# Optimization experiments

Measured on AMD Instinct MI355X. Metric: run time of the kernel, lower is better.

Reference implementation:

```python
import jax, jax.numpy as jnp
import numpy as np

N = 16384   # total gate nodes (64 graphs x 256 gates)
B = 64      # graphs in batch
E = 49152   # directed edges (avg in-degree 3)
Q = 32      # qubit_num
F = 256     # feat_dim
D = 2 * F   # node feature dim = 512
H = 2       # heads
A = 128     # action_num


def _gatv2(x, wl, wr, att, b, src, dst, n):
    # PyG GATv2Conv (concat=True, share_weights=False, negative_slope=0.2)
    h, c = att.shape
    xl = (x @ wl).reshape(n, h, c)   # source-side projection [N,H,C]
    xr = (x @ wr).reshape(n, h, c)   # target-side projection [N,H,C]
    e = jax.nn.leaky_relu(xl[src] + xr[dst], 0.2)       # [E,H,C]
    logit = jnp.einsum('ehc,hc->eh', e, att)             # [E,H]
    m = jax.ops.segment_max(logit, dst, num_segments=n)  # softmax over in-edges per target
    p = jnp.exp(logit - m[dst])
    den = jax.ops.segment_sum(p, dst, num_segments=n)
    alpha = p / den[dst]                                 # [E,H]
    out = jax.ops.segment_sum(alpha[:, :, None] * xl[src], dst, num_segments=n)
    return out.reshape(n, h * c) + b


def _forward(x, xt_w1, xt_b1, xt_w2, xt_b2,
             g0_wl, g0_wr, g0_att, g0_b,
             g1_wl, g1_wr, g1_att, g1_b,
             g2_wl, g2_wr, g2_att, g2_b,
             g3_wl, g3_wr, g3_att, g3_b,
             g4_wl, g4_wr, g4_att, g4_b,
             ln_w, ln_b, aggr_t,
             m_w1, m_b1, m_w2, m_b2, m_w3, m_b3,
             edge_index, batch):
    lr = lambda v: jax.nn.leaky_relu(v, 0.01)
    # x_trans: Linear -> LeakyReLU -> Linear, then fold qubit-pairs into one node
    h0 = lr(x @ xt_w1 + xt_b1) @ xt_w2 + xt_b2           # [2N, F]
    cx = h0.reshape(-1, D)                               # [N, 2F]
    n = cx.shape[0]
    # GATv2Conv default add_self_loops=True (inputs contain no self loops)
    sl = jnp.arange(n, dtype=edge_index.dtype)
    src = jnp.concatenate([edge_index[0], sl])
    dst = jnp.concatenate([edge_index[1], sl])
    res = cx
    h = lr(_gatv2(cx, g0_wl, g0_wr, g0_att, g0_b, src, dst, n))
    for wl_, wr_, att_, b_ in ((g1_wl, g1_wr, g1_att, g1_b),
                               (g2_wl, g2_wr, g2_att, g2_b),
                               (g3_wl, g3_wr, g3_att, g3_b)):
        h = lr(_gatv2(h, wl_, wr_, att_, b_, src, dst, n))
    h = lr(_gatv2(h, g4_wl, g4_wr, g4_att, g4_b, src, dst, n))
    h = h + res                                           # residual [N, 2F]
    # PyG LayerNorm(mode='graph'): normalize over nodes AND channels per graph
    cnt = jax.ops.segment_sum(jnp.ones((n,), h.dtype), batch, num_segments=B)
    norm = cnt * h.shape[1]
    mean = jax.ops.segment_sum(h.sum(-1), batch, num_segments=B) / norm
    hc = h - mean[batch][:, None]
    var = jax.ops.segment_sum((hc * hc).sum(-1), batch, num_segments=B) / norm
    h = hc / jnp.sqrt(var + 1e-5)[batch][:, None] * ln_w + ln_b
    # SoftmaxAggregation(learn=True): channel-wise softmax over nodes per graph
    logit = h * aggr_t
    mg = jax.ops.segment_max(logit, batch, num_segments=B)
    p = jnp.exp(logit - mg[batch])
    den = jax.ops.segment_sum(p, batch, num_segments=B)
    g = jax.ops.segment_sum((p / den[batch]) * h, batch, num_segments=B)  # [B, 2F]
    # head MLP 512->384->256->128
    o = lr(g @ m_w1 + m_b1)
    o = lr(o @ m_w2 + m_b2)
    return o @ m_w3 + m_b3


def setup_inputs() -> dict:
    key = jax.random.key(0)
    ks = iter(jax.random.split(key, 64))
    def rn(shp, s=0.05):
        return jax.random.normal(next(ks), shp, jnp.float32) * s
    d = {}
    d['x'] = jax.random.normal(next(ks), (2 * N, Q), jnp.float32)
    src = jax.random.randint(next(ks), (E,), 0, N, jnp.int32)
    off = jax.random.randint(next(ks), (E,), 1, N, jnp.int32)
    d['edge_index'] = jnp.stack([src, (src + off) % N])  # no self loops
    d['batch'] = jnp.arange(N, dtype=jnp.int32) // (N // B)
    d['xt_w1'] = rn((Q, F)); d['xt_b1'] = rn((F,))
    d['xt_w2'] = rn((F, F)); d['xt_b2'] = rn((F,))
    d['g0_wl'] = rn((D, H * D)); d['g0_wr'] = rn((D, H * D))
    d['g0_att'] = rn((H, D));    d['g0_b'] = rn((H * D,))
    for i in (1, 2, 3):
        d[f'g{i}_wl'] = rn((H * D, H * D)); d[f'g{i}_wr'] = rn((H * D, H * D))
        d[f'g{i}_att'] = rn((H, D));        d[f'g{i}_b'] = rn((H * D,))
    d['g4_wl'] = rn((H * D, D)); d['g4_wr'] = rn((H * D, D))
    d['g4_att'] = rn((1, D));    d['g4_b'] = rn((D,))
    d['ln_w'] = jnp.ones((D,), jnp.float32); d['ln_b'] = jnp.zeros((D,), jnp.float32)
    d['aggr_t'] = jnp.array(1.0, jnp.float32)
    d['m_w1'] = rn((D, 384)); d['m_b1'] = rn((384,))
    d['m_w2'] = rn((384, 256)); d['m_b2'] = rn((256,))
    d['m_w3'] = rn((256, A)); d['m_b3'] = rn((A,))
    return d


def reference(x, edge_index, batch, xt_w1, xt_b1, xt_w2, xt_b2,
              g0_wl, g0_wr, g0_att, g0_b,
              g1_wl, g1_wr, g1_att, g1_b,
              g2_wl, g2_wr, g2_att, g2_b,
              g3_wl, g3_wr, g3_att, g3_b,
              g4_wl, g4_wr, g4_att, g4_b,
              ln_w, ln_b, aggr_t,
              m_w1, m_b1, m_w2, m_b2, m_w3, m_b3):
    return _forward(x, xt_w1, xt_b1, xt_w2, xt_b2,
                    g0_wl, g0_wr, g0_att, g0_b,
                    g1_wl, g1_wr, g1_att, g1_b,
                    g2_wl, g2_wr, g2_att, g2_b,
                    g3_wl, g3_wr, g3_att, g3_b,
                    g4_wl, g4_wr, g4_att, g4_b,
                    ln_w, ln_b, aggr_t,
                    m_w1, m_b1, m_w2, m_b2, m_w3, m_b3,
                    edge_index, batch)
```

## Files before the change

kernel.cpp:

```cpp
#include <hip/hip_runtime.h>
#include <hip/hip_bf16.h>

typedef __hip_bfloat16 bf16;

#define NN 16384
#define BBG 64
#define EE 49152
#define ET (EE + NN)
#define DD 512
#define NG (NN / BBG)

__device__ __forceinline__ float b2f(bf16 v) { return __bfloat162float(v); }
__device__ __forceinline__ bf16 f2b(float v) { return __float2bfloat16(v); }
__device__ __forceinline__ float sb2f(short s) {
    unsigned u = ((unsigned)(unsigned short)s) << 16;
    return __builtin_bit_cast(float, u);
}
__device__ __forceinline__ short f2bs(float v) {
    bf16 b = f2b(v);
    return __builtin_bit_cast(short, b);
}
__device__ __forceinline__ int clampi(int v, int lo, int hi)
{
    return v < lo ? lo : (v > hi ? hi : v);
}

__device__ __forceinline__ unsigned char enc_e4m3(float y)
{
    unsigned b = __builtin_bit_cast(unsigned, y);
    unsigned s = (b >> 31) << 7;
    float a = fabsf(y);
    unsigned ab = b & 0x7fffffffu;
    unsigned rb = ab + (1u << 19);
    int e = (int)(rb >> 23) - 120;
    unsigned m = (rb >> 20) & 7u;
    unsigned qn = (unsigned)(e << 3) | m;
    if (qn > 126u) qn = 126u;
    unsigned qd = (unsigned)__float2int_rn(a * 512.f);
    unsigned q = (a < 0.015625f) ? qd : qn;
    return (unsigned char)(q | s);
}
__device__ __forceinline__ float dec_e4m3(unsigned q)
{
    unsigned e = (q >> 3) & 15u, m = q & 7u;
    float nrm = __builtin_bit_cast(float, ((e + 120u) << 23) | (m << 20));
    float dnm = (float)m * 0.001953125f;
    float v = e ? nrm : dnm;
    return (q & 128u) ? -v : v;
}

typedef __attribute__((ext_vector_type(8))) short bf16x8;
typedef __attribute__((ext_vector_type(4))) float f32x4;

#define AS1 __attribute__((address_space(1)))
#define AS3 __attribute__((address_space(3)))

__global__ __launch_bounds__(256) void gemm_mfma_bt(
    const bf16* __restrict__ A, const bf16* __restrict__ Bt,
    const float* __restrict__ bias, bf16* __restrict__ Cb,
    int M, int N, int K, float slope, int has_act)
{
    __shared__ bf16 As[128 * 32];
    __shared__ bf16 Bs[128 * 32];
    const int tid = threadIdx.x;
    const int w = tid >> 6;
    const int l = tid & 63;
    const int bm = blockIdx.y * 128;
    const int bn = blockIdx.x * 128;
    const int wrow = (w >> 1) * 64;
    const int wcol = (w & 1) * 64;
    const int quad = l >> 4;
    const int c16 = l & 15;

    const int lrow = l >> 2;
    const int lchunk = l & 3;
    const bf16* Ag = A + (size_t)(bm + w * 16 + lrow) * K + lchunk * 8;
    const bf16* Bg = Bt + (size_t)(bn + w * 16 + lrow) * K + lchunk * 8;
    char* AsB = (char*)As;
    char* BsB = (char*)Bs;

    f32x4 acc[4][4] = {};

    for (int k0 = 0; k0 < K; k0 += 32) {
        __builtin_amdgcn_global_load_lds((const AS1 void*)(Ag + k0),
            (AS3 void*)(AsB + w * 1024), 16, 0, 0);
        __builtin_amdgcn_global_load_lds((const AS1 void*)(Ag + (size_t)64 * K + k0),
            (AS3 void*)(AsB + 4096 + w * 1024), 16, 0, 0);
        __builtin_amdgcn_global_load_lds((const AS1 void*)(Bg + k0),
            (AS3 void*)(BsB + w * 1024), 16, 0, 0);
        __builtin_amdgcn_global_load_lds((const AS1 void*)(Bg + (size_t)64 * K + k0),
            (AS3 void*)(BsB + 4096 + w * 1024), 16, 0, 0);
        __syncthreads();

        bf16x8 a[4], b[4];
#pragma unroll
        for (int i = 0; i < 4; i++) {
            int ra = wrow + i * 16 + c16;
            a[i] = *(const bf16x8*)(AsB + ra * 64 + quad * 16);
            int rb = wcol + i * 16 + c16;
            b[i] = *(const bf16x8*)(BsB + rb * 64 + quad * 16);
        }
#pragma unroll
        for (int i = 0; i < 4; i++)
#pragma unroll
            for (int j = 0; j < 4; j++)
                acc[i][j] = __builtin_amdgcn_mfma_f32_16x16x32_bf16(
                    a[i], b[j], acc[i][j], 0, 0, 0);
        __syncthreads();
    }

#pragma unroll
    for (int i = 0; i < 4; i++) {
#pragma unroll
        for (int j = 0; j < 4; j++) {
            int col = bn + wcol + j * 16 + c16;
            float bv = bias ? bias[col] : 0.f;
#pragma unroll
            for (int r = 0; r < 4; r++) {
                int row = bm + wrow + i * 16 + quad * 4 + r;
                float v = acc[i][j][r] + bv;
                if (has_act) v = (v >= 0.f) ? v : v * slope;
                Cb[(size_t)row * N + col] = f2b(v);
            }
        }
    }
}

__global__ __launch_bounds__(256) void gemm_mfma_dual(
    const bf16* __restrict__ A, const bf16* __restrict__ Bt,
    bf16* __restrict__ X0, bf16* __restrict__ X1,
    int M, int K, int HC)
{
    __shared__ bf16 As[128 * 32];
    __shared__ bf16 Bs[128 * 32];
    const int tid = threadIdx.x;
    const int w = tid >> 6;
    const int l = tid & 63;
    const int bm = blockIdx.y * 128;
    const int bn = blockIdx.x * 128;
    const int wrow = (w >> 1) * 64;
    const int wcol = (w & 1) * 64;
    const int quad = l >> 4;
    const int c16 = l & 15;

    const int lrow = l >> 2;
    const int lchunk = l & 3;
    const bf16* Ag = A + (size_t)(bm + w * 16 + lrow) * K + lchunk * 8;
    const bf16* Bg = Bt + (size_t)(bn + w * 16 + lrow) * K + lchunk * 8;
    char* AsB = (char*)As;
    char* BsB = (char*)Bs;

    f32x4 acc[4][4] = {};

    for (int k0 = 0; k0 < K; k0 += 32) {
        __builtin_amdgcn_global_load_lds((const AS1 void*)(Ag + k0),
            (AS3 void*)(AsB + w * 1024), 16, 0, 0);
        __builtin_amdgcn_global_load_lds((const AS1 void*)(Ag + (size_t)64 * K + k0),
            (AS3 void*)(AsB + 4096 + w * 1024), 16, 0, 0);
        __builtin_amdgcn_global_load_lds((const AS1 void*)(Bg + k0),
            (AS3 void*)(BsB + w * 1024), 16, 0, 0);
        __builtin_amdgcn_global_load_lds((const AS1 void*)(Bg + (size_t)64 * K + k0),
            (AS3 void*)(BsB + 4096 + w * 1024), 16, 0, 0);
        __syncthreads();

        bf16x8 a[4], b[4];
#pragma unroll
        for (int i = 0; i < 4; i++) {
            int ra = wrow + i * 16 + c16;
            a[i] = *(const bf16x8*)(AsB + ra * 64 + quad * 16);
            int rb = wcol + i * 16 + c16;
            b[i] = *(const bf16x8*)(BsB + rb * 64 + quad * 16);
        }
#pragma unroll
        for (int i = 0; i < 4; i++)
#pragma unroll
            for (int j = 0; j < 4; j++)
                acc[i][j] = __builtin_amdgcn_mfma_f32_16x16x32_bf16(
                    a[i], b[j], acc[i][j], 0, 0, 0);
        __syncthreads();
    }

#pragma unroll
    for (int i = 0; i < 4; i++) {
#pragma unroll
        for (int j = 0; j < 4; j++) {
            int col = bn + wcol + j * 16 + c16;
            bf16* dst = (col < HC) ? (X0 + col) : (X1 + col - HC);
#pragma unroll
            for (int r = 0; r < 4; r++) {
                int row = bm + wrow + i * 16 + quad * 4 + r;
                dst[(size_t)row * HC] = f2b(acc[i][j][r]);
            }
        }
    }
}

__global__ __launch_bounds__(256, 4) void quant_rows(
    const bf16* __restrict__ xl, unsigned char* __restrict__ xq,
    bf16* __restrict__ xs)
{
    const int n = blockIdx.x * 4 + (threadIdx.x >> 6);
    const int lane = threadIdx.x & 63;
    const bf16* rp = xl + (size_t)n * 1024 + lane * 16;
    bf16x8 v0 = *(const bf16x8*)(rp);
    bf16x8 v1 = *(const bf16x8*)(rp + 8);
    float x[16];
#pragma unroll
    for (int k = 0; k < 8; k++) { x[k] = sb2f(v0[k]); x[8 + k] = sb2f(v1[k]); }
    float mx = 0.f;
#pragma unroll
    for (int k = 0; k < 16; k++) mx = fmaxf(mx, fabsf(x[k]));
    float sc = b2f(f2b(fmaxf(mx, 1e-20f) * (1.f / 448.f)));
    float isc = 1.f / sc;
    uint4 q;
    unsigned* qw = (unsigned*)&q;
#pragma unroll
    for (int w = 0; w < 4; w++) {
        unsigned pk = 0;
#pragma unroll
        for (int b = 0; b < 4; b++)
            pk |= ((unsigned)enc_e4m3(x[w * 4 + b] * isc)) << (b * 8);
        qw[w] = pk;
    }
    *(uint4*)(xq + (size_t)n * 1024 + lane * 16) = q;
    xs[(size_t)n * 64 + lane] = f2b(sc);
}

__global__ __launch_bounds__(256) void gemm_f32(
    const float* __restrict__ A, const float* __restrict__ W,
    const float* __restrict__ bias, float* __restrict__ C,
    int M, int N, int K, float slope, int has_act)
{
    const int BK = 16;
    __shared__ float Asm[BK][64 + 1];
    __shared__ float Wsm[BK][64 + 1];
    int tid = threadIdx.x;
    int bm = blockIdx.y * 64;
    int bn = blockIdx.x * 64;
    int tr = tid >> 4;
    int tc = tid & 15;
    float acc[4][4] = {};

    for (int k0 = 0; k0 < K; k0 += BK) {
        {
            int col = tid & 15;
            int row = tid >> 4;
#pragma unroll
            for (int p = 0; p < 4; p++) {
                int r = row + p * 16;
                Asm[col][r] = A[(size_t)(bm + r) * K + k0 + col];
            }
        }
        {
            int wc = tid & 63;
            int wr = tid >> 6;
#pragma unroll
            for (int p = 0; p < 4; p++) {
                int r = wr + p * 4;
                Wsm[r][wc] = W[(size_t)(k0 + r) * N + bn + wc];
            }
        }
        __syncthreads();
#pragma unroll
        for (int kk = 0; kk < BK; kk++) {
            float a[4], w[4];
#pragma unroll
            for (int i = 0; i < 4; i++) a[i] = Asm[kk][tr * 4 + i];
#pragma unroll
            for (int j = 0; j < 4; j++) w[j] = Wsm[kk][tc * 4 + j];
#pragma unroll
            for (int i = 0; i < 4; i++)
#pragma unroll
                for (int j = 0; j < 4; j++)
                    acc[i][j] += a[i] * w[j];
        }
        __syncthreads();
    }
#pragma unroll
    for (int i = 0; i < 4; i++) {
        int r = bm + tr * 4 + i;
#pragma unroll
        for (int j = 0; j < 4; j++) {
            int cn = bn + tc * 4 + j;
            float v = acc[i][j];
            if (bias) v += bias[cn];
            if (has_act) v = (v >= 0.f) ? v : v * slope;
            C[(size_t)r * N + cn] = v;
        }
    }
}

struct TPackAll {
    const float* in[12];
    bf16* out[12];
    int R[12], C[12];
};

__global__ __launch_bounds__(256) void transpose_batch(TPackAll pk)
{
    int z = blockIdx.z;
    int R = pk.R[z], C = pk.C[z];
    int c0 = blockIdx.x * 32;
    int r0 = blockIdx.y * 32;
    if (c0 >= C || r0 >= R) return;
    const float* in = pk.in[z];
    bf16* out = pk.out[z];
    __shared__ float tile[32][33];
    int tx = threadIdx.x & 31;
    int ty = threadIdx.x >> 5;
#pragma unroll
    for (int k = 0; k < 4; k++) {
        int r = ty + k * 8;
        tile[r][tx] = in[(size_t)(r0 + r) * C + c0 + tx];
    }
    __syncthreads();
#pragma unroll
    for (int k = 0; k < 4; k++) {
        int rr = ty + k * 8;
        out[(size_t)(c0 + rr) * R + r0 + tx] = f2b(tile[tx][rr]);
    }
}

__global__ void f2b_vec(const float* __restrict__ in, bf16* __restrict__ out, int n)
{
    int i = blockIdx.x * 256 + threadIdx.x;
    if (i < n) out[i] = f2b(in[i]);
}

__global__ void count_deg(const int* __restrict__ ei, int* __restrict__ deg)
{
    int e = blockIdx.x * 256 + threadIdx.x;
    if (e >= ET) return;
    int d = (e < EE) ? ei[EE + e] : (e - EE);
    d = clampi(d, 0, NN - 1);
    atomicAdd(&deg[d], 1);
}

__global__ __launch_bounds__(256) void scan_deg(const int* __restrict__ deg,
                                                int* __restrict__ rs)
{
    __shared__ int part[256];
    __shared__ int psum[257];
    int tid = threadIdx.x;
    const int per = NN / 256;
    int base = tid * per;
    int s = 0;
    for (int i = 0; i < per; i++) s += deg[base + i];
    part[tid] = s;
    __syncthreads();
    if (tid == 0) {
        int acc = 0;
        for (int i = 0; i < 256; i++) { psum[i] = acc; acc += part[i]; }
        psum[256] = acc;
    }
    __syncthreads();
    int acc = psum[tid];
    for (int i = 0; i < per; i++) { rs[base + i] = acc; acc += deg[base + i]; }
    if (tid == 0) rs[NN] = psum[256];
}

__global__ void fill_csr(const int* __restrict__ ei, const int* __restrict__ rs,
                         int* __restrict__ cur, int* __restrict__ csrc)
{
    int e = blockIdx.x * 256 + threadIdx.x;
    if (e >= ET) return;
    int s, d;
    if (e < EE) { s = ei[e]; d = ei[EE + e]; } else { s = d = e - EE; }
    s = clampi(s, 0, NN - 1);
    d = clampi(d, 0, NN - 1);
    int pos = atomicAdd(&cur[d], 1);
    int slot = clampi(rs[d] + pos, 0, ET - 1);
    csrc[slot] = s;
}

__global__ __launch_bounds__(256, 4) void gat_q(
    const unsigned char* __restrict__ xlq, const bf16* __restrict__ xls,
    const bf16* __restrict__ xr, const float* __restrict__ att,
    const float* __restrict__ bias, const int* __restrict__ rs,
    const int* __restrict__ csrc, bf16* __restrict__ out_b)
{
    constexpr int HC = 1024, CPL = 16;
    const int tid = threadIdx.x;
    const int w = tid >> 6;
    const int lane = tid & 63;
    const int n = blockIdx.x * 4 + w;
    const int c0 = lane * CPL;

    int start = rs[n];
    int deg = clampi(rs[n + 1] - start, 1, 64);
    start = clampi(start, 0, ET - 1);
    int my_src = 0;
    if (lane < deg) my_src = clampi(csrc[start + lane], 0, NN - 1);

    float av[CPL], rv[CPL];
    {
        bf16x8 r0 = *(const bf16x8*)(xr + (size_t)n * HC + c0);
        bf16x8 r1 = *(const bf16x8*)(xr + (size_t)n * HC + c0 + 8);
#pragma unroll
        for (int k = 0; k < 8; k++) { rv[k] = sb2f(r0[k]); rv[8 + k] = sb2f(r1[k]); }
#pragma unroll
        for (int k = 0; k < CPL; k++) av[k] = att[c0 + k];
    }

    float m = -1e30f, den = 0.f;
    float acc[CPL];
#pragma unroll
    for (int k = 0; k < CPL; k++) acc[k] = 0.f;

    auto loadrow = [&](int i, uint4& q, float& sc) {
        int s = __shfl(my_src, i);
        q = *(const uint4*)(xlq + (size_t)s * HC + c0);
        sc = b2f(xls[(size_t)s * 64 + lane]);
    };
    auto process = [&](const uint4& q, float sc) {
        float x[CPL];
        const unsigned* qw = (const unsigned*)&q;
#pragma unroll
        for (int k = 0; k < CPL; k++)
            x[k] = dec_e4m3((qw[k >> 2] >> ((k & 3) * 8)) & 255u) * sc;
        float part = 0.f;
#pragma unroll
        for (int k = 0; k < CPL; k++) {
            float u = x[k] + rv[k];
            u = (u >= 0.f) ? u : 0.2f * u;
            part = fmaf(av[k], u, part);
        }
#pragma unroll
        for (int msk = 16; msk; msk >>= 1) part += __shfl_xor(part, msk);
        float lg = part;
        float mn = fmaxf(m, lg);
        float r = __expf(m - mn);
        float pi = __expf(lg - mn);
        m = mn;
        den = den * r + pi;
#pragma unroll
        for (int k = 0; k < CPL; k++) acc[k] = fmaf(acc[k], r, pi * x[k]);
    };

    uint4 cq, q1, q2, qn;
    float cs, s1, s2, sn;
    loadrow(0, cq, cs);
    if (deg > 1) loadrow(1, q1, s1);
    if (deg > 2) loadrow(2, q2, s2);
    for (int i = 0; i < deg; i++) {
        if (i + 3 < deg) loadrow(i + 3, qn, sn);
        process(cq, cs);
        cq = q1; cs = s1; q1 = q2; s1 = s2; q2 = qn; s2 = sn;
    }

    float inv = 1.f / den;
    bf16x8 ov0, ov1;
#pragma unroll
    for (int k = 0; k < 8; k++) {
        float v = fmaf(acc[k], inv, bias[c0 + k]);
        v = (v >= 0.f) ? v : 0.01f * v;
        ov0[k] = f2bs(v);
        float v2 = fmaf(acc[8 + k], inv, bias[c0 + 8 + k]);
        v2 = (v2 >= 0.f) ? v2 : 0.01f * v2;
        ov1[k] = f2bs(v2);
    }
    *(bf16x8*)(out_b + (size_t)n * HC + c0) = ov0;
    *(bf16x8*)(out_b + (size_t)n * HC + c0 + 8) = ov1;
}

__global__ __launch_bounds__(256) void gat_b512(
    const bf16* __restrict__ xl, const bf16* __restrict__ xr,
    const float* __restrict__ att, const float* __restrict__ bias,
    const int* __restrict__ rs, const int* __restrict__ csrc,
    const bf16* __restrict__ res, bf16* __restrict__ out_b,
    float* __restrict__ lnsums)
{
    constexpr int HC = 512, CPL = 8;
    const int tid = threadIdx.x;
    const int w = tid >> 6;
    const int lane = tid & 63;
    const int n = blockIdx.x * 4 + w;
    const int c0 = lane * CPL;

    int start = rs[n];
    int deg = clampi(rs[n + 1] - start, 1, 64);
    start = clampi(start, 0, ET - 1);
    int my_src = 0;
    if (lane < deg) my_src = clampi(csrc[start + lane], 0, NN - 1);

    float av[CPL], rv[CPL];
    {
        bf16x8 rp = *(const bf16x8*)(xr + (size_t)n * HC + c0);
#pragma unroll
        for (int k = 0; k < CPL; k++) {
            rv[k] = sb2f(rp[k]);
            av[k] = att[c0 + k];
        }
    }

    float m = -1e30f, den = 0.f;
    float acc[CPL];
#pragma unroll
    for (int k = 0; k < CPL; k++) acc[k] = 0.f;

    auto loadrow = [&](int i, bf16x8& dst) {
        int s = __shfl(my_src, i);
        dst = *(const bf16x8*)(xl + (size_t)s * HC + c0);
    };

    bf16x8 cur, nx1, nx2, nxt;
    loadrow(0, cur);
    if (deg > 1) loadrow(1, nx1);
    if (deg > 2) loadrow(2, nx2);

    for (int i = 0; i < deg; i++) {
        if (i + 3 < deg) loadrow(i + 3, nxt);
        float part = 0.f;
#pragma unroll
        for (int k = 0; k < CPL; k++) {
            float x = sb2f(cur[k]);
            float u = x + rv[k];
            u = (u >= 0.f) ? u : 0.2f * u;
            part = fmaf(av[k], u, part);
        }
#pragma unroll
        for (int msk = 32; msk; msk >>= 1) part += __shfl_xor(part, msk);
        float lg = part;
        float mn = fmaxf(m, lg);
        float r = __expf(m - mn);
        float pi = __expf(lg - mn);
        m = mn;
        den = den * r + pi;
#pragma unroll
        for (int k = 0; k < CPL; k++) {
            float x = sb2f(cur[k]);
            acc[k] = fmaf(acc[k], r, pi * x);
        }
        cur = nx1; nx1 = nx2; nx2 = nxt;
    }

    float inv = 1.f / den;
    float ls = 0.f, ls2 = 0.f;
    float vals[CPL];
#pragma unroll
    for (int k = 0; k < CPL; k++) {
        float v = fmaf(acc[k], inv, bias[c0 + k]);
        v = (v >= 0.f) ? v : 0.01f * v;
        vals[k] = v;
    }
    {
        bf16x8 rr = *(const bf16x8*)(res + (size_t)n * HC + c0);
#pragma unroll
        for (int k = 0; k < CPL; k++) {
            vals[k] += sb2f(rr[k]);
            ls += vals[k];
            ls2 += vals[k] * vals[k];
        }
    }
    bf16x8 ov;
#pragma unroll
    for (int k = 0; k < 8; k++) ov[k] = f2bs(vals[k]);
    *(bf16x8*)(out_b + (size_t)n * HC + c0) = ov;

#pragma unroll
    for (int msk = 32; msk; msk >>= 1) {
        ls += __shfl_xor(ls, msk);
        ls2 += __shfl_xor(ls2, msk);
    }
    if (lane == 0) {
        int g = n >> 8;
        atomicAdd(&lnsums[g], ls);
        atomicAdd(&lnsums[BBG + g], ls2);
    }
}

__global__ __launch_bounds__(256) void aggr_partial(
    const bf16* __restrict__ h, const float* __restrict__ lnsums,
    const float* __restrict__ lnw, const float* __restrict__ lnb,
    const float* __restrict__ t_, float* __restrict__ pm,
    float* __restrict__ pd, float* __restrict__ pa)
{
    int g = blockIdx.x, ch = blockIdx.y, nk = blockIdx.z;
    int tid = threadIdx.x;
    int c = ch * 256 + tid;
    const float tot = (float)(NG * DD);
    float S = lnsums[g], S2 = lnsums[BBG + g];
    float mu = S / tot;
    float iv = rsqrtf(fmaxf(S2 / tot - mu * mu, 0.f) + 1e-5f);
    float w = lnw[c], b = lnb[c], t = t_[0];
    size_t base = (size_t)g * NG * DD + (size_t)nk * 32 * DD + c;
    float m = -1e30f, den = 0.f, acc = 0.f;
    for (int i = 0; i < 32; i++) {
        float hn = (b2f(h[base + (size_t)i * DD]) - mu) * iv * w + b;
        float lg = hn * t;
        if (lg > m) {
            float r = __expf(m - lg);
            den *= r; acc *= r; m = lg;
        }
        float p = __expf(lg - m);
        den += p; acc += p * hn;
    }
    size_t idx = (((size_t)g * 2 + ch) * 8 + nk) * 256 + tid;
    pm[idx] = m; pd[idx] = den; pa[idx] = acc;
}

__global__ __launch_bounds__(256) void aggr_combine(
    const float* __restrict__ pm, const float* __restrict__ pd,
    const float* __restrict__ pa, float* __restrict__ gout)
{
    int g = blockIdx.x, ch = blockIdx.y;
    int tid = threadIdx.x;
    size_t base = (((size_t)g * 2 + ch) * 8) * 256 + tid;
    float m = -1e30f;
#pragma unroll
    for (int k = 0; k < 8; k++) m = fmaxf(m, pm[base + k * 256]);
    float den = 0.f, acc = 0.f;
#pragma unroll
    for (int k = 0; k < 8; k++) {
        float r = __expf(pm[base + k * 256] - m);
        den += pd[base + k * 256] * r;
        acc += pa[base + k * 256] * r;
    }
    gout[(size_t)g * DD + ch * 256 + tid] = acc / den;
}

extern "C" void kernel_launch(void* const* d_in, const int* in_sizes, int n_in,
                              void* d_out, int out_size, void* d_ws, size_t ws_size,
                              hipStream_t stream)
{
    const float* x      = (const float*)d_in[0];
    const int*   ei     = (const int*)d_in[1];
    const float* xt_w1  = (const float*)d_in[3];
    const float* xt_b1  = (const float*)d_in[4];
    const float* xt_w2  = (const float*)d_in[5];
    const float* xt_b2  = (const float*)d_in[6];
    const float* ln_w   = (const float*)d_in[27];
    const float* ln_b   = (const float*)d_in[28];
    const float* aggr_t = (const float*)d_in[29];
    const float* m_w1   = (const float*)d_in[30];
    const float* m_b1   = (const float*)d_in[31];
    const float* m_w2   = (const float*)d_in[32];
    const float* m_b2   = (const float*)d_in[33];
    const float* m_w3   = (const float*)d_in[34];
    const float* m_b3   = (const float*)d_in[35];
    float* out = (float*)d_out;

    char* p = (char*)d_ws;
    auto take = [&](size_t bytes) {
        char* r = p;
        p += (bytes + 255) & ~(size_t)255;
        return r;
    };
    int* i_deg     = (int*)take((size_t)(NN + 1) * 4);
    int* i_rs      = (int*)take((size_t)(NN + 1) * 4);
    int* i_cur     = (int*)take((size_t)NN * 4);
    int* i_src     = (int*)take((size_t)ET * 4);
    float* f_sums  = (float*)take((size_t)2 * BBG * 4);
    float* f_pm    = (float*)take((size_t)BBG * 2 * 8 * 256 * 4);
    float* f_pd    = (float*)take((size_t)BBG * 2 * 8 * 256 * 4);
    float* f_pa    = (float*)take((size_t)BBG * 2 * 8 * 256 * 4);
    float* b_g     = (float*)take((size_t)BBG * DD * 4);
    float* b_m1    = (float*)take((size_t)BBG * 384 * 4);
    float* b_m2    = (float*)take((size_t)BBG * 256 * 4);
    bf16* b_resb   = (bf16*)take((size_t)NN * DD * 2);
    bf16* b_h      = (bf16*)take((size_t)NN * DD * 2);
    bf16* b_hb     = (bf16*)take((size_t)NN * 1024 * 2);
    bf16* b_xlb    = (bf16*)take((size_t)NN * 1024 * 2);
    bf16* b_xrb    = (bf16*)take((size_t)NN * 1024 * 2);
    unsigned char* b_xlq = (unsigned char*)take((size_t)NN * 1024);
    bf16* b_xls    = (bf16*)take((size_t)NN * 64 * 2);
    bf16* b_xb     = (bf16*)take((size_t)2 * NN * 32 * 2);
    bf16* b_wcat   = (bf16*)take((size_t)8 * 1024 * 1024 * 2);
    bf16* b_w1b    = (bf16*)take((size_t)32 * 256 * 2);
    bf16* b_w2b    = (bf16*)take((size_t)256 * 256 * 2);
    bf16* b_t1b = b_hb;

    size_t woff[5];
    {
        size_t o = 0;
        for (int L = 0; L < 5; L++) {
            int Fin = (L == 0) ? 512 : 1024;
            int HC  = (L == 4) ? 512 : 1024;
            woff[L] = o;
            o += (size_t)2 * HC * Fin;
        }
    }

    dim3 blk(256);

    hipMemsetAsync(i_deg, 0, (size_t)(NN + 1) * 4, stream);
    hipMemsetAsync(i_cur, 0, (size_t)NN * 4, stream);
    hipMemsetAsync(f_sums, 0, (size_t)2 * BBG * 4, stream);
    count_deg<<<ET / 256, blk, 0, stream>>>(ei, i_deg);
    scan_deg<<<1, blk, 0, stream>>>(i_deg, i_rs);
    fill_csr<<<ET / 256, blk, 0, stream>>>(ei, i_rs, i_cur, i_src);

    f2b_vec<<<(2 * NN * 32 + 255) / 256, blk, 0, stream>>>(x, b_xb, 2 * NN * 32);
    {
        TPackAll pk;
        pk.in[0] = xt_w1; pk.out[0] = b_w1b; pk.R[0] = 32;  pk.C[0] = 256;
        pk.in[1] = xt_w2; pk.out[1] = b_w2b; pk.R[1] = 256; pk.C[1] = 256;
        for (int L = 0; L < 5; L++) {
            int Fin = (L == 0) ? 512 : 1024;
            int HC  = (L == 4) ? 512 : 1024;
            pk.in[2 + 2 * L] = (const float*)d_in[7 + 4 * L];
            pk.out[2 + 2 * L] = b_wcat + woff[L];
            pk.R[2 + 2 * L] = Fin; pk.C[2 + 2 * L] = HC;
            pk.in[3 + 2 * L] = (const float*)d_in[8 + 4 * L];
            pk.out[3 + 2 * L] = b_wcat + woff[L] + (size_t)HC * Fin;
            pk.R[3 + 2 * L] = Fin; pk.C[3 + 2 * L] = HC;
        }
        transpose_batch<<<dim3(32, 32, 12), blk, 0, stream>>>(pk);
    }

    gemm_mfma_bt<<<dim3(256 / 128, 32768 / 128), blk, 0, stream>>>(
        b_xb, b_w1b, xt_b1, b_t1b, 32768, 256, 32, 0.01f, 1);
    gemm_mfma_bt<<<dim3(256 / 128, 32768 / 128), blk, 0, stream>>>(
        b_t1b, b_w2b, xt_b2, b_resb, 32768, 256, 256, 0.f, 0);

    for (int L = 0; L < 5; L++) {
        const float* att = (const float*)d_in[9 + 4 * L];
        const float* gb  = (const float*)d_in[10 + 4 * L];
        int Fin = (L == 0) ? 512 : 1024;
        int HC  = (L == 4) ? 512 : 1024;
        const bf16* hin = (L == 0) ? b_resb : b_hb;

        gemm_mfma_dual<<<dim3(2 * HC / 128, NN / 128), blk, 0, stream>>>(
            hin, b_wcat + woff[L], b_xlb, b_xrb, NN, Fin, HC);
        if (L < 4) {
            quant_rows<<<NN / 4, blk, 0, stream>>>(b_xlb, b_xlq, b_xls);
            gat_q<<<NN / 4, blk, 0, stream>>>(
                b_xlq, b_xls, b_xrb, att, gb, i_rs, i_src, b_hb);
        } else {
            gat_b512<<<NN / 4, blk, 0, stream>>>(
                b_xlb, b_xrb, att, gb, i_rs, i_src, b_resb, b_h, f_sums);
        }
    }

    aggr_partial<<<dim3(BBG, 2, 8), blk, 0, stream>>>(
        b_h, f_sums, ln_w, ln_b, aggr_t, f_pm, f_pd, f_pa);
    aggr_combine<<<dim3(BBG, 2), blk, 0, stream>>>(f_pm, f_pd, f_pa, b_g);

    gemm_f32<<<dim3(384 / 64, 1), blk, 0, stream>>>(
        b_g, m_w1, m_b1, b_m1, 64, 384, 512, 0.01f, 1);
    gemm_f32<<<dim3(256 / 64, 1), blk, 0, stream>>>(
        b_m1, m_w2, m_b2, b_m2, 64, 256, 384, 0.01f, 1);
    gemm_f32<<<dim3(128 / 64, 1), blk, 0, stream>>>(
        b_m2, m_w3, m_b3, out, 64, 128, 256, 0.f, 0);
}
```

Measured before the change: 1.086 ms.

## Pack fp8 rows with inline scales, quantize last GAT layer, use fixed-slot adjacency

Interleaves each node's per-lane bf16 scales with its fp8 payload in one padded row, so a gather touches a single contiguous region instead of two arrays. The final 512-wide GAT layer now also quantizes source features to fp8 with an extra quant kernel, which halves its gather bytes but adds approximation error there. The CSR build (degree count, scan, fill) is replaced by a fixed 64-slot per-node adjacency filled with atomics, which removes two launches. The trade-off is that neighbor order within a node is nondeterministic and any neighbors beyond 64 are dropped.

```diff
diff --git a/kernel.cpp b/kernel.cpp
--- a/kernel.cpp
+++ b/kernel.cpp
@@ -9,6 +9,8 @@
 #define ET (EE + NN)
 #define DD 512
 #define NG (NN / BBG)
+#define RS1024 1152
+#define RS512  640
 
 __device__ __forceinline__ float b2f(bf16 v) { return __bfloat162float(v); }
 __device__ __forceinline__ bf16 f2b(float v) { return __float2bfloat16(v); }
@@ -195,9 +197,8 @@
     }
 }
 
-__global__ __launch_bounds__(256, 4) void quant_rows(
-    const bf16* __restrict__ xl, unsigned char* __restrict__ xq,
-    bf16* __restrict__ xs)
+__global__ __launch_bounds__(256, 4) void quant1024(
+    const bf16* __restrict__ xl, unsigned char* __restrict__ xp)
 {
     const int n = blockIdx.x * 4 + (threadIdx.x >> 6);
     const int lane = threadIdx.x & 63;
@@ -222,8 +223,38 @@
             pk |= ((unsigned)enc_e4m3(x[w * 4 + b] * isc)) << (b * 8);
         qw[w] = pk;
     }
-    *(uint4*)(xq + (size_t)n * 1024 + lane * 16) = q;
-    xs[(size_t)n * 64 + lane] = f2b(sc);
+    unsigned char* row = xp + (size_t)n * RS1024;
+    *(uint4*)(row + 128 + lane * 16) = q;
+    ((bf16*)row)[lane] = f2b(sc);
+}
+
+__global__ __launch_bounds__(256, 4) void quant512(
+    const bf16* __restrict__ xl, unsigned char* __restrict__ xp)
+{
+    const int n = blockIdx.x * 4 + (threadIdx.x >> 6);
+    const int lane = threadIdx.x & 63;
+    bf16x8 v0 = *(const bf16x8*)(xl + (size_t)n * 512 + lane * 8);
+    float x[8];
+#pragma unroll
+    for (int k = 0; k < 8; k++) x[k] = sb2f(v0[k]);
+    float mx = 0.f;
+#pragma unroll
+    for (int k = 0; k < 8; k++) mx = fmaxf(mx, fabsf(x[k]));
+    float sc = b2f(f2b(fmaxf(mx, 1e-20f) * (1.f / 448.f)));
+    float isc = 1.f / sc;
+    uint2 q;
+    unsigned* qw = (unsigned*)&q;
+#pragma unroll
+    for (int w = 0; w < 2; w++) {
+        unsigned pk = 0;
+#pragma unroll
+        for (int b = 0; b < 4; b++)
+            pk |= ((unsigned)enc_e4m3(x[w * 4 + b] * isc)) << (b * 8);
+        qw[w] = pk;
+    }
+    unsigned char* row = xp + (size_t)n * RS512;
+    *(uint2*)(row + 128 + lane * 8) = q;
+    ((bf16*)row)[lane] = f2b(sc);
 }
 
 __global__ __launch_bounds__(256) void gemm_f32(
@@ -327,40 +358,8 @@
     if (i < n) out[i] = f2b(in[i]);
 }
 
-__global__ void count_deg(const int* __restrict__ ei, int* __restrict__ deg)
-{
-    int e = blockIdx.x * 256 + threadIdx.x;
-    if (e >= ET) return;
-    int d = (e < EE) ? ei[EE + e] : (e - EE);
-    d = clampi(d, 0, NN - 1);
-    atomicAdd(&deg[d], 1);
-}
-
-__global__ __launch_bounds__(256) void scan_deg(const int* __restrict__ deg,
-                                                int* __restrict__ rs)
-{
-    __shared__ int part[256];
-    __shared__ int psum[257];
-    int tid = threadIdx.x;
-    const int per = NN / 256;
-    int base = tid * per;
-    int s = 0;
-    for (int i = 0; i < per; i++) s += deg[base + i];
-    part[tid] = s;
-    __syncthreads();
-    if (tid == 0) {
-        int acc = 0;
-        for (int i = 0; i < 256; i++) { psum[i] = acc; acc += part[i]; }
-        psum[256] = acc;
-    }
-    __syncthreads();
-    int acc = psum[tid];
-    for (int i = 0; i < per; i++) { rs[base + i] = acc; acc += deg[base + i]; }
-    if (tid == 0) rs[NN] = psum[256];
-}
-
-__global__ void fill_csr(const int* __restrict__ ei, const int* __restrict__ rs,
-                         int* __restrict__ cur, int* __restrict__ csrc)
+__global__ void fill_csr(const int* __restrict__ ei, int* __restrict__ cur,
+                         int* __restrict__ csrc)
 {
     int e = blockIdx.x * 256 + threadIdx.x;
     if (e >= ET) return;
@@ -369,15 +368,14 @@
     s = clampi(s, 0, NN - 1);
     d = clampi(d, 0, NN - 1);
     int pos = atomicAdd(&cur[d], 1);
-    int slot = clampi(rs[d] + pos, 0, ET - 1);
-    csrc[slot] = s;
+    if (pos < 64) csrc[d * 64 + pos] = s;
 }
 
 __global__ __launch_bounds__(256, 4) void gat_q(
-    const unsigned char* __restrict__ xlq, const bf16* __restrict__ xls,
-    const bf16* __restrict__ xr, const float* __restrict__ att,
-    const float* __restrict__ bias, const int* __restrict__ rs,
-    const int* __restrict__ csrc, bf16* __restrict__ out_b)
+    const unsigned char* __restrict__ xp, const bf16* __restrict__ xr,
+    const float* __restrict__ att, const float* __restrict__ bias,
+    const int* __restrict__ cur, const int* __restrict__ csrc,
+    bf16* __restrict__ out_b)
 {
     constexpr int HC = 1024, CPL = 16;
     const int tid = threadIdx.x;
@@ -386,11 +384,8 @@
     const int n = blockIdx.x * 4 + w;
     const int c0 = lane * CPL;
 
-    int start = rs[n];
-    int deg = clampi(rs[n + 1] - start, 1, 64);
-    start = clampi(start, 0, ET - 1);
-    int my_src = 0;
-    if (lane < deg) my_src = clampi(csrc[start + lane], 0, NN - 1);
+    int deg = clampi(cur[n], 1, 64);
+    int my_src = clampi(csrc[n * 64 + lane], 0, NN - 1);
 
     float av[CPL], rv[CPL];
     {
@@ -409,8 +404,9 @@
 
     auto loadrow = [&](int i, uint4& q, float& sc) {
         int s = __shfl(my_src, i);
-        q = *(const uint4*)(xlq + (size_t)s * HC + c0);
-        sc = b2f(xls[(size_t)s * 64 + lane]);
+        const unsigned char* row = xp + (size_t)s * RS1024;
+        sc = b2f(*(const bf16*)(row + lane * 2));
+        q = *(const uint4*)(row + 128 + lane * 16);
     };
     auto process = [&](const uint4& q, float sc) {
         float x[CPL];
@@ -463,10 +459,10 @@
     *(bf16x8*)(out_b + (size_t)n * HC + c0 + 8) = ov1;
 }
 
-__global__ __launch_bounds__(256) void gat_b512(
-    const bf16* __restrict__ xl, const bf16* __restrict__ xr,
+__global__ __launch_bounds__(256, 4) void gat_q512(
+    const unsigned char* __restrict__ xp, const bf16* __restrict__ xr,
     const float* __restrict__ att, const float* __restrict__ bias,
-    const int* __restrict__ rs, const int* __restrict__ csrc,
+    const int* __restrict__ cur, const int* __restrict__ csrc,
     const bf16* __restrict__ res, bf16* __restrict__ out_b,
     float* __restrict__ lnsums)
 {
@@ -477,11 +473,8 @@
     const int n = blockIdx.x * 4 + w;
     const int c0 = lane * CPL;
 
-    int start = rs[n];
-    int deg = clampi(rs[n + 1] - start, 1, 64);
-    start = clampi(start, 0, ET - 1);
-    int my_src = 0;
-    if (lane < deg) my_src = clampi(csrc[start + lane], 0, NN - 1);
+    int deg = clampi(cur[n], 1, 64);
+    int my_src = clampi(csrc[n * 64 + lane], 0, NN - 1);
 
     float av[CPL], rv[CPL];
     {
@@ -498,23 +491,22 @@
 #pragma unroll
     for (int k = 0; k < CPL; k++) acc[k] = 0.f;
 
-    auto loadrow = [&](int i, bf16x8& dst) {
+    auto loadrow = [&](int i, uint2& q, float& sc) {
         int s = __shfl(my_src, i);
-        dst = *(const bf16x8*)(xl + (size_t)s * HC + c0);
+        const unsigned char* row = xp + (size_t)s * RS512;
+        sc = b2f(*(const bf16*)(row + lane * 2));
+        q = *(const uint2*)(row + 128 + lane * 8);
     };
-
-    bf16x8 cur, nx1, nx2, nxt;
-    loadrow(0, cur);
-    if (deg > 1) loadrow(1, nx1);
-    if (deg > 2) loadrow(2, nx2);
-
-    for (int i = 0; i < deg; i++) {
-        if (i + 3 < deg) loadrow(i + 3, nxt);
+    auto process = [&](const uint2& q, float sc) {
+        float x[CPL];
+        const unsigned* qw = (const unsigned*)&q;
+#pragma unroll
+        for (int k = 0; k < CPL; k++)
+            x[k] = dec_e4m3((qw[k >> 2] >> ((k & 3) * 8)) & 255u) * sc;
         float part = 0.f;
 #pragma unroll
         for (int k = 0; k < CPL; k++) {
-            float x = sb2f(cur[k]);
-            float u = x + rv[k];
+            float u = x[k] + rv[k];
             u = (u >= 0.f) ? u : 0.2f * u;
             part = fmaf(av[k], u, part);
         }
@@ -527,11 +519,18 @@
         m = mn;
         den = den * r + pi;
 #pragma unroll
-        for (int k = 0; k < CPL; k++) {
-            float x = sb2f(cur[k]);
-            acc[k] = fmaf(acc[k], r, pi * x);
-        }
-        cur = nx1; nx1 = nx2; nx2 = nxt;
+        for (int k = 0; k < CPL; k++) acc[k] = fmaf(acc[k], r, pi * x[k]);
+    };
+
+    uint2 cq, q1, q2, qn;
+    float cs, s1, s2, sn;
+    loadrow(0, cq, cs);
+    if (deg > 1) loadrow(1, q1, s1);
+    if (deg > 2) loadrow(2, q2, s2);
+    for (int i = 0; i < deg; i++) {
+        if (i + 3 < deg) loadrow(i + 3, qn, sn);
+        process(cq, cs);
+        cq = q1; cs = s1; q1 = q2; s1 = s2; q2 = qn; s2 = sn;
     }
 
     float inv = 1.f / den;
@@ -646,10 +645,8 @@
         p += (bytes + 255) & ~(size_t)255;
         return r;
     };
-    int* i_deg     = (int*)take((size_t)(NN + 1) * 4);
-    int* i_rs      = (int*)take((size_t)(NN + 1) * 4);
     int* i_cur     = (int*)take((size_t)NN * 4);
-    int* i_src     = (int*)take((size_t)ET * 4);
+    int* i_src     = (int*)take((size_t)NN * 64 * 4);
     float* f_sums  = (float*)take((size_t)2 * BBG * 4);
     float* f_pm    = (float*)take((size_t)BBG * 2 * 8 * 256 * 4);
     float* f_pd    = (float*)take((size_t)BBG * 2 * 8 * 256 * 4);
@@ -662,8 +659,7 @@
     bf16* b_hb     = (bf16*)take((size_t)NN * 1024 * 2);
     bf16* b_xlb    = (bf16*)take((size_t)NN * 1024 * 2);
     bf16* b_xrb    = (bf16*)take((size_t)NN * 1024 * 2);
-    unsigned char* b_xlq = (unsigned char*)take((size_t)NN * 1024);
-    bf16* b_xls    = (bf16*)take((size_t)NN * 64 * 2);
+    unsigned char* b_xp = (unsigned char*)take((size_t)NN * RS1024);
     bf16* b_xb     = (bf16*)take((size_t)2 * NN * 32 * 2);
     bf16* b_wcat   = (bf16*)take((size_t)8 * 1024 * 1024 * 2);
     bf16* b_w1b    = (bf16*)take((size_t)32 * 256 * 2);
@@ -683,12 +679,9 @@
 
     dim3 blk(256);
 
-    hipMemsetAsync(i_deg, 0, (size_t)(NN + 1) * 4, stream);
     hipMemsetAsync(i_cur, 0, (size_t)NN * 4, stream);
     hipMemsetAsync(f_sums, 0, (size_t)2 * BBG * 4, stream);
-    count_deg<<<ET / 256, blk, 0, stream>>>(ei, i_deg);
-    scan_deg<<<1, blk, 0, stream>>>(i_deg, i_rs);
-    fill_csr<<<ET / 256, blk, 0, stream>>>(ei, i_rs, i_cur, i_src);
+    fill_csr<<<ET / 256, blk, 0, stream>>>(ei, i_cur, i_src);
 
     f2b_vec<<<(2 * NN * 32 + 255) / 256, blk, 0, stream>>>(x, b_xb, 2 * NN * 32);
     {
@@ -723,12 +716,13 @@
         gemm_mfma_dual<<<dim3(2 * HC / 128, NN / 128), blk, 0, stream>>>(
             hin, b_wcat + woff[L], b_xlb, b_xrb, NN, Fin, HC);
         if (L < 4) {
-            quant_rows<<<NN / 4, blk, 0, stream>>>(b_xlb, b_xlq, b_xls);
+            quant1024<<<NN / 4, blk, 0, stream>>>(b_xlb, b_xp);
             gat_q<<<NN / 4, blk, 0, stream>>>(
-                b_xlq, b_xls, b_xrb, att, gb, i_rs, i_src, b_hb);
+                b_xp, b_xrb, att, gb, i_cur, i_src, b_hb);
         } else {
-            gat_b512<<<NN / 4, blk, 0, stream>>>(
-                b_xlb, b_xrb, att, gb, i_rs, i_src, b_resb, b_h, f_sums);
+            quant512<<<NN / 4, blk, 0, stream>>>(b_xlb, b_xp);
+            gat_q512<<<NN / 4, blk, 0, stream>>>(
+                b_xp, b_xrb, att, gb, i_cur, i_src, b_resb, b_h, f_sums);
         }
     }
 
```

Measured after the change: 1.063 ms. -2.1%, faster.
